# Optimization experiments

Measured on AMD Instinct MI355X. Metric: run time of the kernel, lower is better.

Reference implementation:

```python
import jax, jax.numpy as jnp
import numpy as np

D = 4096
K = 128
N = 8192
EPS = 1e-6


def setup_inputs() -> dict:
    key = jax.random.key(0)
    k1, k2 = jax.random.split(key)
    x = jax.random.normal(k1, (N, D), dtype=jnp.float32)
    # theta = [W (d*K), mu (d), sigma (d), alpha (K)]; sigma/alpha must be positive
    theta = jax.random.uniform(k2, (D * K + 2 * D + K,), dtype=jnp.float32)
    return {"x": x, "theta": theta, "full_data_size": 100000}


def reference(x, theta, full_data_size):
    W = theta[: D * K].reshape(D, K)
    mu = theta[D * K : D * K + D]
    sigma = theta[D * K + D : D * K + 2 * D]
    alpha = theta[D * K + 2 * D :]

    # W_multiplied = W * alpha (broadcast over columns)
    Wm = W * alpha  # [D, K]
    # var_noise = sigma * eye(D) + eps : diag(sigma) plus eps added to EVERY entry
    cov = Wm @ Wm.T + jnp.diag(sigma) + EPS  # [D, D]

    L = jnp.linalg.cholesky(cov)  # [D, D], lower
    diff = x - mu  # [N, D]
    # Solve L y = diff^T for all samples at once
    y = jax.scipy.linalg.solve_triangular(L, diff.T, lower=True)  # [D, N]
    quad = jnp.sum(y * y, axis=0)  # [N]
    logdet = 2.0 * jnp.sum(jnp.log(jnp.diagonal(L)))
    log2pi = jnp.float32(np.log(2.0 * np.pi))
    logp = -0.5 * (D * log2pi + logdet + quad)  # [N]

    n = x.shape[0]
    return jnp.sum(logp) * (full_data_size / n)
```

## Files before the change

kernel.cpp:

```cpp
#include <hip/hip_runtime.h>
#include <math.h>

#define D 4096
#define K 128
#define KP 129
#define NC 144
#define NROWS 8192
#define QS 144
#define MS 132
#define NP 132
#define NPS 136
#define NB 12
#define NPAN (NP / NB)
#define MSPLIT 3
#define NTRACE 45
#define LOG2PI 1.8378770664093453

typedef __attribute__((ext_vector_type(8))) short bh8;
typedef __attribute__((ext_vector_type(4))) float f32x4;

__device__ __forceinline__ unsigned short f2bf(float f) {
  unsigned int u = __float_as_uint(f);
  unsigned int r = u + 0x7FFFu + ((u >> 16) & 1u);
  return (unsigned short)(r >> 16);
}
__device__ __forceinline__ float bf2f(unsigned short u) {
  return __uint_as_float(((unsigned int)u) << 16);
}
__device__ __forceinline__ float blo(unsigned int v) { return __uint_as_float(v << 16); }
__device__ __forceinline__ float bhi(unsigned int v) { return __uint_as_float(v & 0xFFFF0000u); }

__device__ __forceinline__ float blockReduceSum256(float v) {
  #pragma unroll
  for (int off = 32; off > 0; off >>= 1) v += __shfl_down(v, off, 64);
  __shared__ float tmp[4];
  __syncthreads();
  if ((threadIdx.x & 63) == 0) tmp[threadIdx.x >> 6] = v;
  __syncthreads();
  float r = 0.0f;
  if (threadIdx.x == 0) r = tmp[0] + tmp[1] + tmp[2] + tmp[3];
  return r;
}

__device__ __forceinline__ float blockReduceSum512(float v) {
  #pragma unroll
  for (int off = 32; off > 0; off >>= 1) v += __shfl_down(v, off, 64);
  __shared__ float tmp8[8];
  __syncthreads();
  if ((threadIdx.x & 63) == 0) tmp8[threadIdx.x >> 6] = v;
  __syncthreads();
  float r = 0.0f;
  if (threadIdx.x == 0) {
    #pragma unroll
    for (int i = 0; i < 8; ++i) r += tmp8[i];
  }
  return r;
}

__global__ __launch_bounds__(256) void k_prep(const float* __restrict__ theta,
                                              unsigned short* __restrict__ VbT) {
  int c = blockIdx.x;
  const float* sg = theta + (size_t)D * K + D;
  float al = (c < K) ? theta[(size_t)D * K + 2 * D + c] : 0.0f;
  for (int d = threadIdx.x; d < D; d += 256) {
    float v;
    if (c < K)       v = theta[(size_t)d * K + c] * al / sg[d];
    else if (c == K) v = 1.0e-3f / sg[d];
    else             v = 0.0f;
    VbT[(size_t)c * D + d] = f2bf(v);
  }
}

__global__ __launch_bounds__(256) void k_M(const float* __restrict__ theta,
                                           const unsigned short* __restrict__ VbT,
                                           float* __restrict__ M) {
  int j = blockIdx.x, kk2 = blockIdx.y;
  if (kk2 < j) return;
  const float* sg = theta + (size_t)D * K + D;
  float acc = 0.0f;
  for (int d0 = threadIdx.x * 8; d0 < D; d0 += 2048) {
    uint4 ua = *reinterpret_cast<const uint4*>(&VbT[(size_t)j * D + d0]);
    uint4 ub = *reinterpret_cast<const uint4*>(&VbT[(size_t)kk2 * D + d0]);
    float4 s0 = *reinterpret_cast<const float4*>(&sg[d0]);
    float4 s1 = *reinterpret_cast<const float4*>(&sg[d0 + 4]);
    acc += s0.x * blo(ua.x) * blo(ub.x) + s0.y * bhi(ua.x) * bhi(ub.x)
         + s0.z * blo(ua.y) * blo(ub.y) + s0.w * bhi(ua.y) * bhi(ub.y)
         + s1.x * blo(ua.z) * blo(ub.z) + s1.y * bhi(ua.z) * bhi(ub.z)
         + s1.z * blo(ua.w) * blo(ub.w) + s1.w * bhi(ua.w) * bhi(ub.w);
  }
  float r = blockReduceSum256(acc);
  if (threadIdx.x == 0) {
    float m = r + (j == kk2 ? 1.0f : 0.0f);
    M[j * MS + kk2] = m;
    M[kk2 * MS + j] = m;
  }
}

#define GBM 32
#define GBK 128
#define NSTEP (D / GBK)
#define XSS 136
#define GEMM_BLOCKS (NROWS / GBM)
#define CS_BLOCKS 32
#define CS_ROWS (NROWS / CS_BLOCKS)

struct CholSh {
  float A[NP][NPS];
  float GT[NP][NPS];
  float Tst[NPAN][NB][NB + 1];
};
struct GemmSh {
  unsigned short Xs[GBM][XSS];
  unsigned short Vs[NC][XSS];
};
union ParSh {
  CholSh c;
  GemmSh g;
};

__device__ void chol_body(CholSh& sh, const float* __restrict__ Mg,
                          float* __restrict__ Gg, float* __restrict__ scalars) {
  auto& A = sh.A;
  auto& GT = sh.GT;
  auto& Tst = sh.Tst;
  __shared__ float redB[8];
  int tid = threadIdx.x;

  for (int idx = tid; idx < NP * NP; idx += 512) {
    int r = idx / NP, c = idx - r * NP;
    A[r][c] = (r < KP && c < KP) ? Mg[r * MS + c] : (r == c ? 1.0f : 0.0f);
  }
  {
    float* gt = &GT[0][0];
    for (int idx = tid; idx < NP * NPS; idx += 512) gt[idx] = 0.0f;
  }
  __syncthreads();

  for (int p = 0; p < NPAN; ++p) {
    int j0 = p * NB, j1 = j0 + NB;
    int nbrows = NP - j1;
    int nG = p * NB;
    if (tid < 128) {
      float T[NB][NB];
      #pragma unroll
      for (int r = 0; r < NB; ++r)
        #pragma unroll
        for (int c = 0; c <= r; ++c)
          T[r][c] = A[j0 + r][j0 + c];
      float dinv[NB];
      #pragma unroll
      for (int jj = 0; jj < NB; ++jj) {
        float dv = sqrtf(T[jj][jj]);
        float iv = 1.0f / dv;
        dinv[jj] = iv;
        #pragma unroll
        for (int r = jj + 1; r < NB; ++r) T[r][jj] *= iv;
        #pragma unroll
        for (int cc = jj + 1; cc < NB; ++cc)
          #pragma unroll
          for (int r = cc; r < NB; ++r)
            T[r][cc] -= T[r][jj] * T[cc][jj];
      }
      #pragma unroll
      for (int r = 0; r < NB; ++r) {
        float tmp[NB];
        #pragma unroll
        for (int c = 0; c < r; ++c) {
          float s = 0.0f;
          #pragma unroll
          for (int k = c; k < r; ++k) s += T[r][k] * T[k][c];
          tmp[c] = -s * dinv[r];
        }
        #pragma unroll
        for (int c = 0; c < r; ++c) T[r][c] = tmp[c];
        T[r][r] = dinv[r];
      }
      if (tid == 0) {
        #pragma unroll
        for (int c = 0; c < NB; ++c) {
          float g[NB];
          #pragma unroll
          for (int r = 0; r < NB; ++r) g[r] = (r >= c) ? T[r][c] : 0.0f;
          float4* dst = reinterpret_cast<float4*>(&GT[j0 + c][j0]);
          float4 g0 = {g[0], g[1], g[2], g[3]};
          float4 g1 = {g[4], g[5], g[6], g[7]};
          float4 g2 = {g[8], g[9], g[10], g[11]};
          dst[0] = g0; dst[1] = g1; dst[2] = g2;
        }
      }
      if (tid < nbrows) {
        int r = j1 + tid;
        float* arow = &A[r][j0];
        float4 q0 = *reinterpret_cast<const float4*>(arow);
        float4 q1 = *reinterpret_cast<const float4*>(arow + 4);
        float4 q2 = *reinterpret_cast<const float4*>(arow + 8);
        float ro[NB] = {q0.x, q0.y, q0.z, q0.w, q1.x, q1.y, q1.z, q1.w,
                        q2.x, q2.y, q2.z, q2.w};
        float rn[NB];
        #pragma unroll
        for (int cc = 0; cc < NB; ++cc) {
          float s = 0.0f;
          #pragma unroll
          for (int k = 0; k <= cc; ++k) s += ro[k] * T[cc][k];
          rn[cc] = s;
        }
        float4 w0 = {rn[0], rn[1], rn[2], rn[3]};
        float4 w1 = {rn[4], rn[5], rn[6], rn[7]};
        float4 w2 = {rn[8], rn[9], rn[10], rn[11]};
        *reinterpret_cast<float4*>(arow) = w0;
        *reinterpret_cast<float4*>(arow + 4) = w1;
        *reinterpret_cast<float4*>(arow + 8) = w2;
      }
    } else if (tid < 128 + MSPLIT * nG) {
      int t2 = tid - 128;
      int q = t2 / (NB * MSPLIT);
      int rem = t2 - q * (NB * MSPLIT);
      int j = rem % NB, mg = rem / NB;
      int qI = q * NB;
      int m0 = mg * 4;
      float t0 = 0.0f, t1 = 0.0f, t2a = 0.0f, t3 = 0.0f;
      for (int k = q; k < p; ++k) {
        int kI = k * NB;
        const float* gp = &GT[qI + j][kI];
        float4 g0 = *reinterpret_cast<const float4*>(gp);
        float4 g1 = *reinterpret_cast<const float4*>(gp + 4);
        float4 g2 = *reinterpret_cast<const float4*>(gp + 8);
        #pragma unroll
        for (int i = 0; i < 4; ++i) {
          const float* ap = &A[j0 + m0 + i][kI];
          float4 a0 = *reinterpret_cast<const float4*>(ap);
          float4 a1 = *reinterpret_cast<const float4*>(ap + 4);
          float4 a2 = *reinterpret_cast<const float4*>(ap + 8);
          float s = a0.x * g0.x + a0.y * g0.y + a0.z * g0.z + a0.w * g0.w
                  + a1.x * g1.x + a1.y * g1.y + a1.z * g1.z + a1.w * g1.w
                  + a2.x * g2.x + a2.y * g2.y + a2.z * g2.z + a2.w * g2.w;
          if (i == 0) t0 += s;
          else if (i == 1) t1 += s;
          else if (i == 2) t2a += s;
          else t3 += s;
        }
      }
      Tst[q][m0 + 0][j] = t0;
      Tst[q][m0 + 1][j] = t1;
      Tst[q][m0 + 2][j] = t2a;
      Tst[q][m0 + 3][j] = t3;
    }
    __syncthreads();
    if (tid < nG) {
      int q = tid / NB, j = tid - (tid / NB) * NB;
      int qI = q * NB;
      float w[NB];
      #pragma unroll
      for (int m = 0; m < NB; ++m) w[m] = Tst[q][m][j];
      float rn[NB];
      #pragma unroll
      for (int i = 0; i < NB; ++i) {
        float s = 0.0f;
        #pragma unroll
        for (int m = 0; m <= i; ++m) s += GT[j0 + m][j0 + i] * w[m];
        rn[i] = -s;
      }
      float4* dst = reinterpret_cast<float4*>(&GT[qI + j][j0]);
      float4 r0 = {rn[0], rn[1], rn[2], rn[3]};
      float4 r1 = {rn[4], rn[5], rn[6], rn[7]};
      float4 r2 = {rn[8], rn[9], rn[10], rn[11]};
      dst[0] = r0; dst[1] = r1; dst[2] = r2;
    } else {
      int nt = nbrows / 4;
      int ntasks = nt * (nt + 1) / 2;
      int nthr = 512 - nG;
      for (int t = tid - nG; t < ntasks; t += nthr) {
        int r4 = (int)((sqrtf(8.0f * (float)t + 1.0f) - 1.0f) * 0.5f);
        while ((r4 + 1) * (r4 + 2) / 2 <= t) ++r4;
        while (r4 * (r4 + 1) / 2 > t) --r4;
        int c4 = t - r4 * (r4 + 1) / 2;
        int r = j1 + r4 * 4, c = j1 + c4 * 4;
        float pr[4][NB], pc[4][NB];
        #pragma unroll
        for (int i = 0; i < 4; ++i) {
          float4 a0 = *reinterpret_cast<const float4*>(&A[r + i][j0]);
          float4 a1 = *reinterpret_cast<const float4*>(&A[r + i][j0 + 4]);
          float4 a2 = *reinterpret_cast<const float4*>(&A[r + i][j0 + 8]);
          pr[i][0] = a0.x; pr[i][1] = a0.y; pr[i][2] = a0.z; pr[i][3] = a0.w;
          pr[i][4] = a1.x; pr[i][5] = a1.y; pr[i][6] = a1.z; pr[i][7] = a1.w;
          pr[i][8] = a2.x; pr[i][9] = a2.y; pr[i][10] = a2.z; pr[i][11] = a2.w;
          float4 b0 = *reinterpret_cast<const float4*>(&A[c + i][j0]);
          float4 b1 = *reinterpret_cast<const float4*>(&A[c + i][j0 + 4]);
          float4 b2 = *reinterpret_cast<const float4*>(&A[c + i][j0 + 8]);
          pc[i][0] = b0.x; pc[i][1] = b0.y; pc[i][2] = b0.z; pc[i][3] = b0.w;
          pc[i][4] = b1.x; pc[i][5] = b1.y; pc[i][6] = b1.z; pc[i][7] = b1.w;
          pc[i][8] = b2.x; pc[i][9] = b2.y; pc[i][10] = b2.z; pc[i][11] = b2.w;
        }
        float4 av[4];
        #pragma unroll
        for (int i = 0; i < 4; ++i)
          av[i] = *reinterpret_cast<const float4*>(&A[r + i][c]);
        #pragma unroll
        for (int k = 0; k < NB; ++k) {
          #pragma unroll
          for (int i = 0; i < 4; ++i) {
            av[i].x -= pr[i][k] * pc[0][k];
            av[i].y -= pr[i][k] * pc[1][k];
            av[i].z -= pr[i][k] * pc[2][k];
            av[i].w -= pr[i][k] * pc[3][k];
          }
        }
        #pragma unroll
        for (int i = 0; i < 4; ++i)
          *reinterpret_cast<float4*>(&A[r + i][c]) = av[i];
      }
    }
    __syncthreads();
  }

  for (int idx = tid; idx < NP * NP; idx += 512) {
    int r = idx / NP, c = idx - r * NP;
    Gg[idx] = GT[r][c];
  }

  float lg = (tid < NP) ? logf(GT[tid][tid]) : 0.0f;
  #pragma unroll
  for (int off = 32; off > 0; off >>= 1) lg += __shfl_down(lg, off, 64);
  __syncthreads();
  if ((tid & 63) == 0) redB[tid >> 6] = lg;
  __syncthreads();
  if (tid == 0) {
    float sgl = 0.0f;
    #pragma unroll
    for (int i = 0; i < 8; ++i) sgl += redB[i];
    scalars[2] = -2.0f * sgl;
  }
}

__device__ void gemm_body(GemmSh& sh, const float* __restrict__ x,
                          const unsigned short* __restrict__ VbT,
                          unsigned short* __restrict__ Yb,
                          float* __restrict__ tvec, int blk) {
  auto& Xs = sh.Xs;
  auto& Vs = sh.Vs;
  int tid = threadIdx.x;
  int row0 = blk * GBM;
  int wid = tid >> 6, lane = tid & 63;
  int lr = lane & 15, lk = (lane >> 4) * 8;
  int rt = wid & 1;
  int cg = wid >> 1;
  int ct0 = (cg == 0) ? 0 : (cg * 2 + 1);
  int nct = (cg == 0) ? 3 : 2;

  int sxr = tid >> 4;
  int sxk = (tid & 15) * 8;
  int vrb = tid >> 4;
  int vk  = (tid & 15) * 8;

  float4 xr0, xr1;
  uint4 vr0, vr1, vr2, vr3, vr4;
  {
    const float* xb = &x[(size_t)(row0 + sxr) * D + sxk];
    xr0 = *reinterpret_cast<const float4*>(xb);
    xr1 = *reinterpret_cast<const float4*>(xb + 4);
    const unsigned short* vb = &VbT[(size_t)vrb * D + vk];
    vr0 = *reinterpret_cast<const uint4*>(vb);
    vr1 = *reinterpret_cast<const uint4*>(vb + (size_t)32 * D);
    vr2 = *reinterpret_cast<const uint4*>(vb + (size_t)64 * D);
    vr3 = *reinterpret_cast<const uint4*>(vb + (size_t)96 * D);
    if (tid < 256) vr4 = *reinterpret_cast<const uint4*>(vb + (size_t)128 * D);
  }

  f32x4 acc0 = {0, 0, 0, 0}, acc1 = {0, 0, 0, 0}, acc2 = {0, 0, 0, 0};

  for (int s = 0; s < NSTEP; ++s) {
    {
      uint4 w;
      w.x = (unsigned)f2bf(xr0.x) | ((unsigned)f2bf(xr0.y) << 16);
      w.y = (unsigned)f2bf(xr0.z) | ((unsigned)f2bf(xr0.w) << 16);
      w.z = (unsigned)f2bf(xr1.x) | ((unsigned)f2bf(xr1.y) << 16);
      w.w = (unsigned)f2bf(xr1.z) | ((unsigned)f2bf(xr1.w) << 16);
      *reinterpret_cast<uint4*>(&Xs[sxr][sxk]) = w;
      unsigned short* vd = &Vs[vrb][vk];
      *reinterpret_cast<uint4*>(vd) = vr0;
      *reinterpret_cast<uint4*>(vd + 32 * XSS) = vr1;
      *reinterpret_cast<uint4*>(vd + 64 * XSS) = vr2;
      *reinterpret_cast<uint4*>(vd + 96 * XSS) = vr3;
      if (tid < 256) *reinterpret_cast<uint4*>(vd + 128 * XSS) = vr4;
    }
    __syncthreads();
    if (s + 1 < NSTEP) {
      const float* xb = &x[(size_t)(row0 + sxr) * D + (s + 1) * GBK + sxk];
      xr0 = *reinterpret_cast<const float4*>(xb);
      xr1 = *reinterpret_cast<const float4*>(xb + 4);
      const unsigned short* vb = &VbT[(size_t)vrb * D + (s + 1) * GBK + vk];
      vr0 = *reinterpret_cast<const uint4*>(vb);
      vr1 = *reinterpret_cast<const uint4*>(vb + (size_t)32 * D);
      vr2 = *reinterpret_cast<const uint4*>(vb + (size_t)64 * D);
      vr3 = *reinterpret_cast<const uint4*>(vb + (size_t)96 * D);
      if (tid < 256) vr4 = *reinterpret_cast<const uint4*>(vb + (size_t)128 * D);
    }
    #pragma unroll
    for (int ks = 0; ks < 4; ++ks) {
      bh8 a = *reinterpret_cast<const bh8*>(&Xs[rt * 16 + lr][ks * 32 + lk]);
      bh8 b0 = *reinterpret_cast<const bh8*>(&Vs[ct0 * 16 + lr][ks * 32 + lk]);
      acc0 = __builtin_amdgcn_mfma_f32_16x16x32_bf16(a, b0, acc0, 0, 0, 0);
      bh8 b1 = *reinterpret_cast<const bh8*>(&Vs[(ct0 + 1) * 16 + lr][ks * 32 + lk]);
      acc1 = __builtin_amdgcn_mfma_f32_16x16x32_bf16(a, b1, acc1, 0, 0, 0);
      if (nct == 3) {
        bh8 b2 = *reinterpret_cast<const bh8*>(&Vs[(ct0 + 2) * 16 + lr][ks * 32 + lk]);
        acc2 = __builtin_amdgcn_mfma_f32_16x16x32_bf16(a, b2, acc2, 0, 0, 0);
      }
    }
    __syncthreads();
  }

  int rw = row0 + rt * 16 + ((lane >> 4) << 2);
  #pragma unroll
  for (int g = 0; g < 4; ++g)
    Yb[(size_t)(rw + g) * NC + ct0 * 16 + lr] = f2bf(acc0[g]);
  #pragma unroll
  for (int g = 0; g < 4; ++g)
    Yb[(size_t)(rw + g) * NC + (ct0 + 1) * 16 + lr] = f2bf(acc1[g]);
  if (nct == 3) {
    #pragma unroll
    for (int g = 0; g < 4; ++g)
      Yb[(size_t)(rw + g) * NC + (ct0 + 2) * 16 + lr] = f2bf(acc2[g]);
  }

  {
    float c0 = acc0[0] + acc0[1] + acc0[2] + acc0[3];
    c0 += __shfl_xor(c0, 16, 64);
    c0 += __shfl_xor(c0, 32, 64);
    float c1 = acc1[0] + acc1[1] + acc1[2] + acc1[3];
    c1 += __shfl_xor(c1, 16, 64);
    c1 += __shfl_xor(c1, 32, 64);
    float c2 = 0.0f;
    if (nct == 3) {
      c2 = acc2[0] + acc2[1] + acc2[2] + acc2[3];
      c2 += __shfl_xor(c2, 16, 64);
      c2 += __shfl_xor(c2, 32, 64);
    }
    if ((lane >> 4) == 0) {
      atomicAdd(&tvec[ct0 * 16 + lr], c0);
      atomicAdd(&tvec[(ct0 + 1) * 16 + lr], c1);
      if (nct == 3) atomicAdd(&tvec[(ct0 + 2) * 16 + lr], c2);
    }
  }
}

__device__ void colstats_body(const float* __restrict__ x,
                              const float* __restrict__ theta,
                              float* __restrict__ scalars, int cb) {
  int i0 = cb * CS_ROWS;
  const float* mu = theta + (size_t)D * K;
  const float* sg = mu + D;
  int dA = threadIdx.x * 4, dB = (threadIdx.x + 512) * 4;
  float4 muA = *reinterpret_cast<const float4*>(&mu[dA]);
  float4 sgA = *reinterpret_cast<const float4*>(&sg[dA]);
  float4 muB = *reinterpret_cast<const float4*>(&mu[dB]);
  float4 sgB = *reinterpret_cast<const float4*>(&sg[dB]);
  float4 ivA = {1.0f / sgA.x, 1.0f / sgA.y, 1.0f / sgA.z, 1.0f / sgA.w};
  float4 ivB = {1.0f / sgB.x, 1.0f / sgB.y, 1.0f / sgB.z, 1.0f / sgB.w};
  float t1 = 0.0f;
  for (int i = i0; i < i0 + CS_ROWS; ++i) {
    float4 a = *reinterpret_cast<const float4*>(&x[(size_t)i * D + dA]);
    float4 b = *reinterpret_cast<const float4*>(&x[(size_t)i * D + dB]);
    float ax = a.x - muA.x, ay = a.y - muA.y, az = a.z - muA.z, aw = a.w - muA.w;
    float bx = b.x - muB.x, by = b.y - muB.y, bz = b.z - muB.z, bw = b.w - muB.w;
    t1 += ax * ax * ivA.x + ay * ay * ivA.y + az * az * ivA.z + aw * aw * ivA.w;
    t1 += bx * bx * ivB.x + by * by * ivB.y + bz * bz * ivB.z + bw * bw * ivB.w;
  }
  float r = blockReduceSum512(t1);
  if (threadIdx.x == 0) atomicAdd(&scalars[1], r);
  if (cb == 0) {
    float lg = logf(sgA.x) + logf(sgA.y) + logf(sgA.z) + logf(sgA.w)
             + logf(sgB.x) + logf(sgB.y) + logf(sgB.z) + logf(sgB.w);
    float r2 = blockReduceSum512(lg);
    if (threadIdx.x == 0) atomicAdd(&scalars[0], r2);
  }
}

__device__ void mvec_body(const unsigned short* __restrict__ VbT,
                          const float* __restrict__ theta,
                          float* __restrict__ mvec, int c) {
  const float* mu = theta + (size_t)D * K;
  int d = threadIdx.x * 8;
  ushort4 u0 = *reinterpret_cast<const ushort4*>(&VbT[(size_t)c * D + d]);
  ushort4 u1 = *reinterpret_cast<const ushort4*>(&VbT[(size_t)c * D + d + 4]);
  float4 m0 = *reinterpret_cast<const float4*>(&mu[d]);
  float4 m1 = *reinterpret_cast<const float4*>(&mu[d + 4]);
  float a = bf2f(u0.x) * m0.x + bf2f(u0.y) * m0.y + bf2f(u0.z) * m0.z + bf2f(u0.w) * m0.w
          + bf2f(u1.x) * m1.x + bf2f(u1.y) * m1.y + bf2f(u1.z) * m1.z + bf2f(u1.w) * m1.w;
  float r = blockReduceSum512(a);
  if (threadIdx.x == 0) mvec[c] = r;
}

__global__ __launch_bounds__(512, 1) void k_par(const float* __restrict__ x,
                                                const float* __restrict__ theta,
                                                const unsigned short* __restrict__ VbT,
                                                unsigned short* __restrict__ Yb,
                                                const float* __restrict__ Mg,
                                                float* __restrict__ Gg,
                                                float* __restrict__ scalars,
                                                float* __restrict__ tvec,
                                                float* __restrict__ mvec) {
  __shared__ ParSh sh;
  int b = blockIdx.x;
  if (b == 0) {
    chol_body(sh.c, Mg, Gg, scalars);
  } else if (b <= GEMM_BLOCKS) {
    gemm_body(sh.g, x, VbT, Yb, tvec, b - 1);
  } else if (b <= GEMM_BLOCKS + CS_BLOCKS) {
    colstats_body(x, theta, scalars, b - 1 - GEMM_BLOCKS);
  } else {
    mvec_body(VbT, theta, mvec, b - 1 - GEMM_BLOCKS - CS_BLOCKS);
  }
}

#define SYRK_ZSPLIT 16
__global__ __launch_bounds__(256) void k_syrk(const unsigned short* __restrict__ Yb,
                                              float* __restrict__ Q) {
  int bj = blockIdx.x * 16, bk = blockIdx.y * 16;
  if (bk < bj) return;
  __shared__ float Ya[64][17];
  __shared__ float Yc[64][17];
  int i0base = blockIdx.z * (NROWS / SYRK_ZSPLIT);
  int tid = threadIdx.x;
  int tj = tid & 15, tk = tid >> 4;
  int lr = tid >> 2, lc = (tid & 3) * 4;
  float acc = 0.0f;
  for (int i0 = i0base; i0 < i0base + NROWS / SYRK_ZSPLIT; i0 += 64) {
    ushort4 va = *reinterpret_cast<const ushort4*>(&Yb[(size_t)(i0 + lr) * NC + bj + lc]);
    ushort4 vc = *reinterpret_cast<const ushort4*>(&Yb[(size_t)(i0 + lr) * NC + bk + lc]);
    Ya[lr][lc + 0] = bf2f(va.x); Ya[lr][lc + 1] = bf2f(va.y);
    Ya[lr][lc + 2] = bf2f(va.z); Ya[lr][lc + 3] = bf2f(va.w);
    Yc[lr][lc + 0] = bf2f(vc.x); Yc[lr][lc + 1] = bf2f(vc.y);
    Yc[lr][lc + 2] = bf2f(vc.z); Yc[lr][lc + 3] = bf2f(vc.w);
    __syncthreads();
    #pragma unroll
    for (int ii = 0; ii < 64; ++ii) acc += Ya[ii][tj] * Yc[ii][tk];
    __syncthreads();
  }
  atomicAdd(&Q[(bj + tj) * QS + bk + tk], acc);
}

__global__ __launch_bounds__(256) void k_trace(const float* __restrict__ Gg,
                                               const float* __restrict__ Qg,
                                               const float* __restrict__ tvec,
                                               const float* __restrict__ mvec,
                                               float* __restrict__ scalars,
                                               const int* __restrict__ fds,
                                               float* __restrict__ out) {
  int b = blockIdx.x;
  int tkT = (int)((sqrtf(8.0f * (float)b + 1.0f) - 1.0f) * 0.5f);
  while ((tkT + 1) * (tkT + 2) / 2 <= b) ++tkT;
  while (tkT * (tkT + 1) / 2 > b) --tkT;
  int tjT = b - tkT * (tkT + 1) / 2;
  int bj = tjT * 16, bk = tkT * 16;
  int tj = threadIdx.x & 15, tk = threadIdx.x >> 4;
  int j = bj + tj, k = bk + tk;
  float acc = 0.0f;
  if (j <= k && k < NP && j < KP && k < KP) {
    const float* gj = Gg + (size_t)j * NP;
    const float* gk = Gg + (size_t)k * NP;
    float h0 = 0.f, h1 = 0.f;
    #pragma unroll 4
    for (int i4 = 0; i4 < NP / 4; ++i4) {
      float4 a = *reinterpret_cast<const float4*>(gj + i4 * 4);
      float4 c = *reinterpret_cast<const float4*>(gk + i4 * 4);
      h0 += a.x * c.x + a.y * c.y;
      h1 += a.z * c.z + a.w * c.w;
    }
    float h = h0 + h1;
    float tlj = tvec[j], mlj = mvec[j], tlk = tvec[k], mlk = mvec[k];
    float S = Qg[j * QS + k] - tlj * mlk - mlj * tlk + (float)NROWS * mlj * mlk;
    acc = ((j == k) ? 1.0f : 2.0f) * h * S;
  }
  float r = blockReduceSum256(acc);
  if (threadIdx.x == 0) {
    atomicAdd(&scalars[3], r);
    __threadfence();
    unsigned old = atomicAdd(reinterpret_cast<unsigned int*>(scalars + 4), 1u);
    if (old == NTRACE - 1) {
      float tr = atomicAdd(&scalars[3], 0.0f);
      double sumlog  = (double)scalars[0];
      double term1   = (double)scalars[1];
      double logdetM = (double)scalars[2];
      double total = (double)NROWS * (double)D * LOG2PI
                   + (double)NROWS * (sumlog + logdetM)
                   + term1 - (double)tr;
      double scale = (double)fds[0] / (double)NROWS;
      out[0] = (float)(scale * (-0.5) * total);
    }
  }
}

extern "C" void kernel_launch(void* const* d_in, const int* in_sizes, int n_in,
                              void* d_out, int out_size, void* d_ws, size_t ws_size,
                              hipStream_t stream) {
  const float* x     = (const float*)d_in[0];
  const float* theta = (const float*)d_in[1];
  const int*   fds   = (const int*)d_in[2];
  float* out = (float*)d_out;
  float* ws = (float*)d_ws;

  float* Q        = ws;
  float* tvec     = Q + QS * QS;
  float* scalars  = tvec + NC;
  unsigned short* Yb  = (unsigned short*)(scalars + 8);
  unsigned short* VbT = Yb + (size_t)NROWS * NC;
  float* M        = (float*)(VbT + (size_t)NC * D);
  float* mvec     = M + KP * MS;
  float* Gg       = mvec + NC;

  hipMemsetAsync(Q, 0, (size_t)(QS * QS + NC + 8) * sizeof(float), stream);

  k_prep <<<dim3(NC), 256, 0, stream>>>(theta, VbT);
  k_M    <<<dim3(KP, KP), 256, 0, stream>>>(theta, VbT, M);
  k_par  <<<dim3(1 + GEMM_BLOCKS + CS_BLOCKS + KP), 512, 0, stream>>>(
             x, theta, VbT, Yb, M, Gg, scalars, tvec, mvec);
  k_syrk <<<dim3(QS / 16, QS / 16, SYRK_ZSPLIT), 256, 0, stream>>>(Yb, Q);
  k_trace<<<dim3(NTRACE), 256, 0, stream>>>(Gg, Q, tvec, mvec, scalars, fds, out);
}
```

Baseline: 152.6 us.

## Tile k_prep over D with shared-memory transpose and fuse mvec reduction

k_prep now processes 64-row slices of W per block, loading them coalesced into shared memory and writing transposed bf16 VbT with vector stores, instead of one column per block with strided reads of W. The mu-weighted reduction (mvec) is folded into k_prep through shuffle and atomicAdd, which removes the mvec blocks from k_par. mvec moves into the memset-zeroed region so the atomics start from zero. This removes uncoalesced theta reads and some k_par work, at the cost of atomic contention and a nondeterministic summation order.

```diff
diff --git a/kernel.cpp b/kernel.cpp
--- a/kernel.cpp
+++ b/kernel.cpp
@@ -57,17 +57,60 @@
   return r;
 }
 
+#define PD 64
 __global__ __launch_bounds__(256) void k_prep(const float* __restrict__ theta,
-                                              unsigned short* __restrict__ VbT) {
-  int c = blockIdx.x;
-  const float* sg = theta + (size_t)D * K + D;
-  float al = (c < K) ? theta[(size_t)D * K + 2 * D + c] : 0.0f;
-  for (int d = threadIdx.x; d < D; d += 256) {
-    float v;
-    if (c < K)       v = theta[(size_t)d * K + c] * al / sg[d];
-    else if (c == K) v = 1.0e-3f / sg[d];
-    else             v = 0.0f;
-    VbT[(size_t)c * D + d] = f2bf(v);
+                                              unsigned short* __restrict__ VbT,
+                                              float* __restrict__ mvec) {
+  __shared__ float Wt[PD][K + 4];
+  __shared__ float isg[PD], mul[PD], alp[K];
+  int tid = threadIdx.x;
+  int d0 = blockIdx.x * PD;
+  const float* mu = theta + (size_t)D * K;
+  const float* sg = mu + D;
+  const float* al = sg + D;
+
+  #pragma unroll
+  for (int it = 0; it < 8; ++it) {
+    int f4 = tid + it * 256;
+    int base = f4 * 4;
+    int r = base >> 7, c = base & 127;
+    float4 w = *reinterpret_cast<const float4*>(&theta[(size_t)(d0 + r) * K + c]);
+    *reinterpret_cast<float4*>(&Wt[r][c]) = w;
+  }
+  if (tid < PD)            isg[tid] = 1.0f / sg[d0 + tid];
+  else if (tid < 2 * PD)   mul[tid - PD] = mu[d0 + tid - PD];
+  else                     alp[tid - 128] = al[tid - 128];
+  __syncthreads();
+
+  int cl = tid >> 4;
+  int dl = (tid & 15) * 4;
+  for (int pc = 0; pc < 9; ++pc) {
+    int c = pc * 16 + cl;
+    float v0, v1, v2, v3;
+    if (c < K) {
+      float a = alp[c];
+      v0 = Wt[dl + 0][c] * a * isg[dl + 0];
+      v1 = Wt[dl + 1][c] * a * isg[dl + 1];
+      v2 = Wt[dl + 2][c] * a * isg[dl + 2];
+      v3 = Wt[dl + 3][c] * a * isg[dl + 3];
+    } else if (c == K) {
+      v0 = 1.0e-3f * isg[dl + 0];
+      v1 = 1.0e-3f * isg[dl + 1];
+      v2 = 1.0e-3f * isg[dl + 2];
+      v3 = 1.0e-3f * isg[dl + 3];
+    } else {
+      v0 = v1 = v2 = v3 = 0.0f;
+    }
+    ushort4 w;
+    w.x = f2bf(v0); w.y = f2bf(v1); w.z = f2bf(v2); w.w = f2bf(v3);
+    *reinterpret_cast<ushort4*>(&VbT[(size_t)c * D + d0 + dl]) = w;
+    if (c <= K) {
+      float mv = bf2f(w.x) * mul[dl + 0] + bf2f(w.y) * mul[dl + 1]
+               + bf2f(w.z) * mul[dl + 2] + bf2f(w.w) * mul[dl + 3];
+      #pragma unroll
+      for (int o = 8; o > 0; o >>= 1) mv += __shfl_xor(mv, o, 16);
+      if ((tid & 15) == 0) atomicAdd(&mvec[c], mv);
+    }
   }
 }
 
@@ -476,21 +519,6 @@
   }
 }
 
-__device__ void mvec_body(const unsigned short* __restrict__ VbT,
-                          const float* __restrict__ theta,
-                          float* __restrict__ mvec, int c) {
-  const float* mu = theta + (size_t)D * K;
-  int d = threadIdx.x * 8;
-  ushort4 u0 = *reinterpret_cast<const ushort4*>(&VbT[(size_t)c * D + d]);
-  ushort4 u1 = *reinterpret_cast<const ushort4*>(&VbT[(size_t)c * D + d + 4]);
-  float4 m0 = *reinterpret_cast<const float4*>(&mu[d]);
-  float4 m1 = *reinterpret_cast<const float4*>(&mu[d + 4]);
-  float a = bf2f(u0.x) * m0.x + bf2f(u0.y) * m0.y + bf2f(u0.z) * m0.z + bf2f(u0.w) * m0.w
-          + bf2f(u1.x) * m1.x + bf2f(u1.y) * m1.y + bf2f(u1.z) * m1.z + bf2f(u1.w) * m1.w;
-  float r = blockReduceSum512(a);
-  if (threadIdx.x == 0) mvec[c] = r;
-}
-
 __global__ __launch_bounds__(512, 1) void k_par(const float* __restrict__ x,
                                                 const float* __restrict__ theta,
                                                 const unsigned short* __restrict__ VbT,
@@ -498,18 +526,15 @@
                                                 const float* __restrict__ Mg,
                                                 float* __restrict__ Gg,
                                                 float* __restrict__ scalars,
-                                                float* __restrict__ tvec,
-                                                float* __restrict__ mvec) {
+                                                float* __restrict__ tvec) {
   __shared__ ParSh sh;
   int b = blockIdx.x;
   if (b == 0) {
     chol_body(sh.c, Mg, Gg, scalars);
   } else if (b <= GEMM_BLOCKS) {
     gemm_body(sh.g, x, VbT, Yb, tvec, b - 1);
-  } else if (b <= GEMM_BLOCKS + CS_BLOCKS) {
+  } else {
     colstats_body(x, theta, scalars, b - 1 - GEMM_BLOCKS);
-  } else {
-    mvec_body(VbT, theta, mvec, b - 1 - GEMM_BLOCKS - CS_BLOCKS);
   }
 }
 
@@ -603,18 +628,18 @@
   float* Q        = ws;
   float* tvec     = Q + QS * QS;
   float* scalars  = tvec + NC;
-  unsigned short* Yb  = (unsigned short*)(scalars + 8);
+  float* mvec     = scalars + 8;
+  unsigned short* Yb  = (unsigned short*)(mvec + NC);
   unsigned short* VbT = Yb + (size_t)NROWS * NC;
   float* M        = (float*)(VbT + (size_t)NC * D);
-  float* mvec     = M + KP * MS;
-  float* Gg       = mvec + NC;
-
-  hipMemsetAsync(Q, 0, (size_t)(QS * QS + NC + 8) * sizeof(float), stream);
-
-  k_prep <<<dim3(NC), 256, 0, stream>>>(theta, VbT);
+  float* Gg       = M + KP * MS;
+
+  hipMemsetAsync(Q, 0, (size_t)(QS * QS + NC + 8 + NC) * sizeof(float), stream);
+
+  k_prep <<<dim3(D / PD), 256, 0, stream>>>(theta, VbT, mvec);
   k_M    <<<dim3(KP, KP), 256, 0, stream>>>(theta, VbT, M);
-  k_par  <<<dim3(1 + GEMM_BLOCKS + CS_BLOCKS + KP), 512, 0, stream>>>(
-             x, theta, VbT, Yb, M, Gg, scalars, tvec, mvec);
+  k_par  <<<dim3(1 + GEMM_BLOCKS + CS_BLOCKS), 512, 0, stream>>>(
+             x, theta, VbT, Yb, M, Gg, scalars, tvec);
   k_syrk <<<dim3(QS / 16, QS / 16, SYRK_ZSPLIT), 256, 0, stream>>>(Yb, Q);
   k_trace<<<dim3(NTRACE), 256, 0, stream>>>(Gg, Q, tvec, mvec, scalars, fds, out);
 }
```

After: 202.7 us. 1.33x slower.
